# Optimization experiments

Measured on AMD Instinct MI355X. Metric: run time of the kernel, lower is better.

Reference implementation:

```python
import jax, jax.numpy as jnp
import numpy as np

N_NODES = 100000
N_EDGES = 1600000
D_IN, D_HID, D_OUT = 128, 128, 64


def spmm(row, col, val, h, n):
    # y[i] = sum_{e: row[e]==i} val[e] * h[col[e]]  (A_hat @ h with A in COO form)
    return jax.ops.segment_sum(val[:, None] * h[col], row, num_segments=n)


def setup_inputs() -> dict:
    key = jax.random.key(0)
    ks = jax.random.split(key, 7)
    x = jax.random.normal(ks[0], (1, N_NODES, D_IN), dtype=jnp.float32)
    edge_row = jax.random.randint(ks[1], (N_EDGES,), 0, N_NODES, dtype=jnp.int32)
    edge_col = jax.random.randint(ks[2], (N_EDGES,), 0, N_NODES, dtype=jnp.int32)
    edge_val = jax.random.uniform(ks[3], (N_EDGES,), dtype=jnp.float32)
    W0 = jax.random.normal(ks[4], (D_HID, D_IN), dtype=jnp.float32) * 0.05
    W1 = jax.random.normal(ks[5], (D_HID, D_HID), dtype=jnp.float32) * 0.05
    W2 = jax.random.normal(ks[6], (D_OUT, D_HID), dtype=jnp.float32) * 0.05
    return {"x": x, "edge_row": edge_row, "edge_col": edge_col,
            "edge_val": edge_val, "W0": W0, "W1": W1, "W2": W2}


def reference(x, edge_row, edge_col, edge_val, W0, W1, W2):
    B, N, D = x.shape
    n = B * N
    h = x.reshape(n, D)
    # input conv: Linear (no bias) -> SpMM -> ReLU
    h = jax.nn.relu(spmm(edge_row, edge_col, edge_val, h @ W0.T, n))
    # hidden conv with residual: ReLU(A (h W1^T)) + h
    h = jax.nn.relu(spmm(edge_row, edge_col, edge_val, h @ W1.T, n)) + h
    # dropout is identity in eval mode
    out = spmm(edge_row, edge_col, edge_val, h @ W2.T, n)
    return out
```

## Files before the change

kernel.cpp:

```cpp
#include <hip/hip_runtime.h>


typedef unsigned int u32;
typedef unsigned short u16;
typedef __attribute__((ext_vector_type(8))) short bf16x8;
typedef __attribute__((ext_vector_type(4))) float f32x4;

constexpr int NN = 100000;
constexpr int NE = 1600000;
constexpr int RPB = 128;
constexpr int NBUCK = 784;
constexpr int PAD = 100352;
constexpr int BCAP = 2432;
constexpr int EPB = 4096;
constexpr int P1B = (NE + EPB - 1) / EPB;
constexpr int G0B = (NN + 63) / 64;
constexpr int NCB = 13;
constexpr int HB  = 1024;

__device__ __forceinline__ u16 f2bf(float f) {
    u32 x = __float_as_uint(f);
    x += 0x7fffu + ((x >> 16) & 1u);
    return (u16)(x >> 16);
}

__device__ __forceinline__ void wfrag_one(const float* __restrict__ W,
                                          u16* __restrict__ Wf, int total, int i)
{
    if (i < total) {
        const int j    = i & 7;
        const int lane = (i >> 3) & 63;
        const int kc   = (i >> 9) & 3;
        const int ct   = i >> 11;
        const int src  = (ct * 16 + (lane & 15)) * 128 + kc * 32 + (lane >> 4) * 8 + j;
        Wf[i] = f2bf(W[src]);
    }
}

__global__ __launch_bounds__(256)
void wcvt_kernel(const float* __restrict__ W0, const float* __restrict__ W1,
                 const float* __restrict__ W2, u16* __restrict__ wf0,
                 u16* __restrict__ wf1, u16* __restrict__ wf2)
{
    const int i = blockIdx.x * 256 + threadIdx.x;
    wfrag_one(W0, wf0, 128 * 128, i);
    wfrag_one(W1, wf1, 128 * 128, i);
    wfrag_one(W2, wf2, 64 * 128, i);
}

__global__ __launch_bounds__(256)
void k1_kernel(const float* __restrict__ x, const u16* __restrict__ Wf,
               u16* __restrict__ Cb,
               const int* __restrict__ erow, const int* __restrict__ ecol,
               const float* __restrict__ eval,
               int2* __restrict__ part, int* __restrict__ boffs)
{
    __shared__ u16 smem[64 * 136];
    const int tid = threadIdx.x;

    if ((int)blockIdx.x < P1B) {
        int* shist = (int*)smem;
        int* sexcl = shist + HB;
        int* sdat  = sexcl + HB;
        const int blk = blockIdx.x;

        #pragma unroll
        for (int j = 0; j < HB / 256; ++j) shist[j * 256 + tid] = 0;
        __syncthreads();

        const int base = blk * EPB;
        int rr[EPB / 256];
        #pragma unroll
        for (int j = 0; j < EPB / 256; ++j) {
            const int e = base + j * 256 + tid;
            rr[j] = (e < NE) ? erow[e] : -1;
            if (rr[j] >= 0) atomicAdd(&shist[rr[j] >> 7], 1);
        }
        __syncthreads();

        int c[4]; int tsum = 0;
        #pragma unroll
        for (int i = 0; i < 4; ++i) { c[i] = shist[tid * 4 + i]; tsum += c[i]; }
        sdat[tid] = tsum;
        __syncthreads();
        #pragma unroll
        for (int off = 1; off < 256; off <<= 1) {
            const int v = (tid >= off) ? sdat[tid - off] : 0;
            __syncthreads();
            sdat[tid] += v;
            __syncthreads();
        }
        int run = sdat[tid] - tsum;
        #pragma unroll
        for (int i = 0; i < 4; ++i) { sexcl[tid * 4 + i] = run; run += c[i]; }
        __syncthreads();

        for (int b = tid; b < NBUCK; b += 256)
            boffs[(size_t)b * P1B + blk] = sexcl[b];
        if (tid == 0) boffs[(size_t)NBUCK * P1B + blk] = sdat[255];
        __syncthreads();

        #pragma unroll
        for (int j = 0; j < EPB / 256; ++j) {
            const int r = rr[j];
            if (r >= 0) {
                const int e = base + j * 256 + tid;
                const int pos = atomicAdd(&sexcl[r >> 7], 1);
                part[(size_t)blk * EPB + pos] =
                    make_int2(((r & 127) << 17) | ecol[e], __float_as_int(eval[e]));
            }
        }
        return;
    }

    constexpr int RS   = 136;
    constexpr int PADW = 136;
    u16* sA = smem;
    u16* sC = smem;
    const int w    = tid >> 6;
    const int lane = tid & 63;
    const int m    = lane & 15;
    const int q    = lane >> 4;
    const int rowBase = ((int)blockIdx.x - P1B) * 64;

    #pragma unroll
    for (int i = 0; i < 8; ++i) {
        const int g = (i * 256 + tid) * 4;
        const int r = g >> 7, c = g & 127;
        float4 v = make_float4(0.f, 0.f, 0.f, 0.f);
        if (rowBase + r < NN) v = *(const float4*)(x + (size_t)(rowBase + r) * 128 + c);
        u16* d = &sA[r * RS + c];
        d[0] = f2bf(v.x); d[1] = f2bf(v.y); d[2] = f2bf(v.z); d[3] = f2bf(v.w);
    }
    __syncthreads();

    bf16x8 afrag[4];
    #pragma unroll
    for (int kc = 0; kc < 4; ++kc)
        afrag[kc] = *(const bf16x8*)&sA[(w * 16 + m) * RS + kc * 32 + q * 8];
    __syncthreads();

    #pragma unroll
    for (int ct = 0; ct < 8; ++ct) {
        f32x4 acc = {0.f, 0.f, 0.f, 0.f};
        #pragma unroll
        for (int kc = 0; kc < 4; ++kc) {
            const bf16x8 b = *(const bf16x8*)(Wf + (((ct * 4 + kc) * 64) + lane) * 8);
            acc = __builtin_amdgcn_mfma_f32_16x16x32_bf16(afrag[kc], b, acc, 0, 0, 0);
        }
        #pragma unroll
        for (int r = 0; r < 4; ++r)
            sC[(w * 16 + q * 4 + r) * PADW + ct * 16 + m] = f2bf(acc[r]);
    }
    __syncthreads();

    const int g    = lane >> 2;
    const int cb   = (lane & 3) * 32;
    const int grow = rowBase + w * 16 + g;
    if (grow < NN) {
        #pragma unroll
        for (int i = 0; i < 4; ++i) {
            const int4 v = *(const int4*)&sC[(w * 16 + g) * PADW + cb + i * 8];
            *(int4*)(Cb + (size_t)grow * 128 + cb + i * 8) = v;
        }
    }
}

__global__ __launch_bounds__(256)
void part2_kernel(const int* __restrict__ boffs, const int2* __restrict__ part,
                  int* __restrict__ offs, int2* __restrict__ pce)
{
    __shared__ int2 sbuf[BCAP];
    __shared__ int scnt[RPB * NCB];
    __shared__ int slo[512];
    __shared__ int sinc[512];
    __shared__ int sdata[256];
    const int b = blockIdx.x;
    const int tid = threadIdx.x;

    int s0 = 0, s1 = 0;
    for (int k = tid; k < P1B; k += 256) {
        s0 += boffs[(size_t)b * P1B + k];
        s1 += boffs[(size_t)(b + 1) * P1B + k];
    }
    {
        int k = tid;
        int l0 = 0, ln = 0;
        if (k < P1B) {
            l0 = boffs[(size_t)b * P1B + k];
            ln = boffs[(size_t)(b + 1) * P1B + k] - l0;
        }
        slo[k] = l0; sinc[k] = ln;
        k = tid + 256; l0 = 0; ln = 0;
        if (k < P1B) {
            l0 = boffs[(size_t)b * P1B + k];
            ln = boffs[(size_t)(b + 1) * P1B + k] - l0;
        }
        slo[k] = l0; sinc[k] = ln;
    }
    sdata[tid] = s0;
    __syncthreads();
    #pragma unroll
    for (int off = 128; off > 0; off >>= 1) {
        if (tid < off) sdata[tid] += sdata[tid + off];
        __syncthreads();
    }
    const int gb = sdata[0];
    __syncthreads();
    sdata[tid] = s1;
    __syncthreads();
    #pragma unroll
    for (int off = 128; off > 0; off >>= 1) {
        if (tid < off) sdata[tid] += sdata[tid + off];
        __syncthreads();
    }
    const int cnt = sdata[0] - gb;
    __syncthreads();

    for (int j = tid; j < RPB * NCB; j += 256) scnt[j] = 0;
    __syncthreads();

    for (int off = 1; off < 512; off <<= 1) {
        const int v0 = (tid >= off) ? sinc[tid - off] : 0;
        const int v1 = (tid + 256 >= off) ? sinc[tid + 256 - off] : 0;
        __syncthreads();
        sinc[tid]       += v0;
        sinc[tid + 256] += v1;
        __syncthreads();
    }

    for (int i = tid; i < cnt; i += 256) {
        int k = 0;
        #pragma unroll
        for (int step = 256; step > 0; step >>= 1) {
            const int nk = k + step;
            if (nk <= 511 && sinc[nk - 1] <= i) k = nk;
        }
        const int loc = i - (k ? sinc[k - 1] : 0);
        sbuf[i] = part[(size_t)k * EPB + slo[k] + loc];
    }
    __syncthreads();

    for (int i = tid; i < cnt; i += 256) {
        const int xk = sbuf[i].x;
        atomicAdd(&scnt[(((u32)xk) >> 17) * NCB + ((xk & 0x1FFFF) >> 13)], 1);
    }
    __syncthreads();

    int rsum = 0;
    if (tid < RPB) {
        #pragma unroll
        for (int j = 0; j < NCB; ++j) rsum += scnt[tid * NCB + j];
    }
    sdata[tid] = rsum;
    __syncthreads();
    #pragma unroll
    for (int off = 1; off < 256; off <<= 1) {
        const int v = (tid >= off) ? sdata[tid - off] : 0;
        __syncthreads();
        sdata[tid] += v;
        __syncthreads();
    }
    const int excl = sdata[tid] - rsum;
    if (tid < RPB) {
        offs[b * RPB + tid] = gb + excl;
        int run = gb + excl;
        #pragma unroll
        for (int j = 0; j < NCB; ++j) {
            const int c = scnt[tid * NCB + j];
            scnt[tid * NCB + j] = run;
            run += c;
        }
    }
    __syncthreads();

    for (int i = tid; i < cnt; i += 256) {
        const int2 ev = sbuf[i];
        const int pos = atomicAdd(
            &scnt[(((u32)ev.x) >> 17) * NCB + ((ev.x & 0x1FFFF) >> 13)], 1);
        pce[pos] = make_int2(ev.x & 0x1FFFF, ev.y);
    }
}

template<int LPC>
__device__ __forceinline__ void load_row(const u16* p, u32* u) {
    if constexpr (LPC == 8) {
        const uint4 t = *(const uint4*)p;
        u[0] = t.x; u[1] = t.y; u[2] = t.z; u[3] = t.w;
    } else {
        const uint2 t = *(const uint2*)p;
        u[0] = t.x; u[1] = t.y;
    }
}

template<int LPC>
__device__ __forceinline__ void fma_row(float v, const u32* u, float* a) {
    #pragma unroll
    for (int j = 0; j < LPC / 2; ++j) {
        a[2*j]   = fmaf(v, __uint_as_float(u[j] << 16),         a[2*j]);
        a[2*j+1] = fmaf(v, __uint_as_float(u[j] & 0xffff0000u), a[2*j+1]);
    }
}

template<int DO, int MODE>
__global__ __launch_bounds__(256)
void spmm_gemm(const int* __restrict__ offs, const int2* __restrict__ pce,
               const u16* __restrict__ Hb, const u16* __restrict__ Wf,
               const u16* __restrict__ Res, u16* __restrict__ Cb,
               u16* __restrict__ Hout)
{
    constexpr int RS   = 136;
    constexpr int PADW = DO + 8;
    __shared__ u16 smem[16 * 136];
    const int tid = threadIdx.x;
    const int ln  = tid & 15;
    const int rl  = tid >> 4;
    const int row = blockIdx.x * 16 + rl;

    const int s = offs[row];
    const int t = offs[row + 1];
    const u16* hbase = Hb + ln * 8;

    float a0[8], a1[8];
    #pragma unroll
    for (int j = 0; j < 8; ++j) { a0[j] = 0.f; a1[j] = 0.f; }

    for (int e = s; e < t; e += 16) {
        int2 my = make_int2(0, 0);
        if (e + ln < t) my = pce[e + ln];
        const int rem = t - e;
        #pragma unroll
        for (int qd = 0; qd < 4; ++qd) {
            if (qd * 4 < rem) {
                const int c0 = __shfl(my.x, qd * 4 + 0, 16);
                const int v0 = __shfl(my.y, qd * 4 + 0, 16);
                const int c1 = __shfl(my.x, qd * 4 + 1, 16);
                const int v1 = __shfl(my.y, qd * 4 + 1, 16);
                const int c2 = __shfl(my.x, qd * 4 + 2, 16);
                const int v2 = __shfl(my.y, qd * 4 + 2, 16);
                const int c3 = __shfl(my.x, qd * 4 + 3, 16);
                const int v3 = __shfl(my.y, qd * 4 + 3, 16);
                u32 u0[4], u1[4], u2[4], u3[4];
                load_row<8>(hbase + (size_t)c0 * 128, u0);
                load_row<8>(hbase + (size_t)c1 * 128, u1);
                load_row<8>(hbase + (size_t)c2 * 128, u2);
                load_row<8>(hbase + (size_t)c3 * 128, u3);
                fma_row<8>(__int_as_float(v0), u0, a0);
                fma_row<8>(__int_as_float(v1), u1, a1);
                fma_row<8>(__int_as_float(v2), u2, a0);
                fma_row<8>(__int_as_float(v3), u3, a1);
            }
        }
    }
    #pragma unroll
    for (int j = 0; j < 8; ++j) a0[j] = fmaxf(a0[j] + a1[j], 0.f);

    if constexpr (MODE == 2) {
        u32 r[4];
        load_row<8>(Res + (size_t)row * 128 + ln * 8, r);
        #pragma unroll
        for (int j = 0; j < 4; ++j) {
            a0[2*j]   += __uint_as_float(r[j] << 16);
            a0[2*j+1] += __uint_as_float(r[j] & 0xffff0000u);
        }
    }
    u32 o[4];
    #pragma unroll
    for (int j = 0; j < 4; ++j)
        o[j] = (u32)f2bf(a0[2*j]) | ((u32)f2bf(a0[2*j+1]) << 16);
    const uint4 packed = make_uint4(o[0], o[1], o[2], o[3]);
    *(uint4*)&smem[rl * RS + ln * 8] = packed;
    if constexpr (MODE == 1)
        *(uint4*)(Hout + (size_t)row * 128 + ln * 8) = packed;
    __syncthreads();

    constexpr int TPW = DO / 64;
    const int w    = tid >> 6;
    const int lane = tid & 63;
    const int m    = lane & 15;
    const int q    = lane >> 4;

    bf16x8 afrag[4];
    #pragma unroll
    for (int kc = 0; kc < 4; ++kc)
        afrag[kc] = *(const bf16x8*)&smem[m * RS + kc * 32 + q * 8];

    f32x4 acc[TPW];
    #pragma unroll
    for (int tw = 0; tw < TPW; ++tw) {
        const int ct = w * TPW + tw;
        acc[tw] = (f32x4){0.f, 0.f, 0.f, 0.f};
        #pragma unroll
        for (int kc = 0; kc < 4; ++kc) {
            const bf16x8 b = *(const bf16x8*)(Wf + (((ct * 4 + kc) * 64) + lane) * 8);
            acc[tw] = __builtin_amdgcn_mfma_f32_16x16x32_bf16(afrag[kc], b, acc[tw], 0, 0, 0);
        }
    }
    __syncthreads();

    #pragma unroll
    for (int tw = 0; tw < TPW; ++tw) {
        const int ct = w * TPW + tw;
        #pragma unroll
        for (int r = 0; r < 4; ++r)
            smem[(q * 4 + r) * PADW + ct * 16 + m] = f2bf(acc[tw][r]);
    }
    __syncthreads();

    if (DO == 128 || tid < 128) {
        const int g = tid * 8;
        const int r = g / DO;
        const int c = g % DO;
        const int4 v = *(const int4*)&smem[r * PADW + c];
        *(int4*)(Cb + ((size_t)blockIdx.x * 16 + r) * DO + c) = v;
    }
}

__global__ __launch_bounds__(256)
void spmm_out(const int* __restrict__ offs, const int2* __restrict__ pce,
              const u16* __restrict__ Hb, float* __restrict__ Y)
{
    const int ln  = threadIdx.x & 15;
    const int row = blockIdx.x * 16 + (threadIdx.x >> 4);
    if (row >= NN) return;
    const int s = offs[row];
    const int t = offs[row + 1];
    const u16* hbase = Hb + ln * 4;

    float a0[4], a1[4];
    #pragma unroll
    for (int j = 0; j < 4; ++j) { a0[j] = 0.f; a1[j] = 0.f; }

    for (int e = s; e < t; e += 16) {
        int2 my = make_int2(0, 0);
        if (e + ln < t) my = pce[e + ln];
        const int rem = t - e;
        #pragma unroll
        for (int qd = 0; qd < 4; ++qd) {
            if (qd * 4 < rem) {
                const int c0 = __shfl(my.x, qd * 4 + 0, 16);
                const int v0 = __shfl(my.y, qd * 4 + 0, 16);
                const int c1 = __shfl(my.x, qd * 4 + 1, 16);
                const int v1 = __shfl(my.y, qd * 4 + 1, 16);
                const int c2 = __shfl(my.x, qd * 4 + 2, 16);
                const int v2 = __shfl(my.y, qd * 4 + 2, 16);
                const int c3 = __shfl(my.x, qd * 4 + 3, 16);
                const int v3 = __shfl(my.y, qd * 4 + 3, 16);
                u32 u0[2], u1[2], u2[2], u3[2];
                load_row<4>(hbase + (size_t)c0 * 64, u0);
                load_row<4>(hbase + (size_t)c1 * 64, u1);
                load_row<4>(hbase + (size_t)c2 * 64, u2);
                load_row<4>(hbase + (size_t)c3 * 64, u3);
                fma_row<4>(__int_as_float(v0), u0, a0);
                fma_row<4>(__int_as_float(v1), u1, a1);
                fma_row<4>(__int_as_float(v2), u2, a0);
                fma_row<4>(__int_as_float(v3), u3, a1);
            }
        }
    }
    #pragma unroll
    for (int j = 0; j < 4; ++j) a0[j] += a1[j];
    *(float4*)(Y + (size_t)row * 64 + ln * 4) = make_float4(a0[0], a0[1], a0[2], a0[3]);
}

extern "C" void kernel_launch(void* const* d_in, const int* in_sizes, int n_in,
                              void* d_out, int out_size, void* d_ws, size_t ws_size,
                              hipStream_t stream) {
    const float* x    = (const float*)d_in[0];
    const int*   erow = (const int*)  d_in[1];
    const int*   ecol = (const int*)  d_in[2];
    const float* eval = (const float*)d_in[3];
    const float* W0   = (const float*)d_in[4];
    const float* W1   = (const float*)d_in[5];
    const float* W2   = (const float*)d_in[6];
    float* out = (float*)d_out;

    char* p = (char*)d_ws;
    const size_t BUFB = (size_t)NN * 128 * sizeof(u16);
    u16* t0b  = (u16*)p;  p += BUFB;
    u16* t1b  = (u16*)p;  p += BUFB;
    u16* h1b  = (u16*)p;  p += BUFB;
    u16* wf0  = (u16*)p;  p += 128 * 128 * 2;
    u16* wf1  = (u16*)p;  p += 128 * 128 * 2;
    u16* wf2  = (u16*)p;  p += 64 * 128 * 2;
    int* boffs  = (int*)p; p += (size_t)(NBUCK + 1) * P1B * 4;
    int* offs   = (int*)p; p += ((size_t)PAD + 256) * 4;
    int2* part  = (int2*)p; p += (size_t)P1B * EPB * 8;
    int2* pce   = (int2*)p;

    const dim3 blk(256);
    const int rowBlocks = NN / 16;

    wcvt_kernel<<<64, blk, 0, stream>>>(W0, W1, W2, wf0, wf1, wf2);
    k1_kernel  <<<P1B + G0B, blk, 0, stream>>>(x, wf0, t0b, erow, ecol, eval, part, boffs);
    part2_kernel<<<NBUCK, blk, 0, stream>>>(boffs, part, offs, pce);
    spmm_gemm<128, 1><<<rowBlocks, blk, 0, stream>>>(offs, pce, t0b, wf1, nullptr, t1b, h1b);
    spmm_gemm<64, 2><<<rowBlocks, blk, 0, stream>>>(offs, pce, t1b, wf2, h1b, t0b, nullptr);
    spmm_out<<<rowBlocks, blk, 0, stream>>>(offs, pce, t0b, out);
}
```

Before: 319.1 us.

## Widen row buckets to 256, transpose bucket offsets, drop column sub-sort

Edge partitioning now uses 256-row buckets (392 buckets) instead of 128-row buckets, halving the number of part2 blocks and doubling per-block shared capacity. The boffs table is transposed to block-major so phase-1 writes are contiguous, and part2 derives the bucket total from the scan instead of a second reduction. The per-row column sub-bucketing (NCB) is removed, so edges within a row are no longer sorted by column range. This cuts preprocessing work but may reduce gather locality in the SpMM kernels. Larger BCAP risks overflow if a bucket exceeds 4608 edges (expected ~4096).

```diff
diff --git a/kernel.cpp b/kernel.cpp
--- a/kernel.cpp
+++ b/kernel.cpp
@@ -8,15 +8,14 @@
 
 constexpr int NN = 100000;
 constexpr int NE = 1600000;
-constexpr int RPB = 128;
-constexpr int NBUCK = 784;
+constexpr int RPB = 256;
+constexpr int NBUCK = 392;
 constexpr int PAD = 100352;
-constexpr int BCAP = 2432;
+constexpr int BCAP = 4608;
 constexpr int EPB = 4096;
 constexpr int P1B = (NE + EPB - 1) / EPB;
 constexpr int G0B = (NN + 63) / 64;
-constexpr int NCB = 13;
-constexpr int HB  = 1024;
+constexpr int BOS = NBUCK + 1;
 
 __device__ __forceinline__ u16 f2bf(float f) {
     u32 x = __float_as_uint(f);
@@ -60,12 +59,10 @@
 
     if ((int)blockIdx.x < P1B) {
         int* shist = (int*)smem;
-        int* sexcl = shist + HB;
-        int* sdat  = sexcl + HB;
+        int* sexcl = shist + 512;
+        int* sdat  = sexcl + 512;
         const int blk = blockIdx.x;
-
-        #pragma unroll
-        for (int j = 0; j < HB / 256; ++j) shist[j * 256 + tid] = 0;
+        shist[tid] = 0; shist[tid + 256] = 0;
         __syncthreads();
 
         const int base = blk * EPB;
@@ -74,13 +71,13 @@
         for (int j = 0; j < EPB / 256; ++j) {
             const int e = base + j * 256 + tid;
             rr[j] = (e < NE) ? erow[e] : -1;
-            if (rr[j] >= 0) atomicAdd(&shist[rr[j] >> 7], 1);
-        }
-        __syncthreads();
-
-        int c[4]; int tsum = 0;
-        #pragma unroll
-        for (int i = 0; i < 4; ++i) { c[i] = shist[tid * 4 + i]; tsum += c[i]; }
+            if (rr[j] >= 0) atomicAdd(&shist[rr[j] >> 8], 1);
+        }
+        __syncthreads();
+
+        const int c0 = shist[2 * tid];
+        const int c1 = shist[2 * tid + 1];
+        const int tsum = c0 + c1;
         sdat[tid] = tsum;
         __syncthreads();
         #pragma unroll
@@ -90,14 +87,14 @@
             sdat[tid] += v;
             __syncthreads();
         }
-        int run = sdat[tid] - tsum;
-        #pragma unroll
-        for (int i = 0; i < 4; ++i) { sexcl[tid * 4 + i] = run; run += c[i]; }
+        const int excl = sdat[tid] - tsum;
+        sexcl[2 * tid]     = excl;
+        sexcl[2 * tid + 1] = excl + c0;
         __syncthreads();
 
         for (int b = tid; b < NBUCK; b += 256)
-            boffs[(size_t)b * P1B + blk] = sexcl[b];
-        if (tid == 0) boffs[(size_t)NBUCK * P1B + blk] = sdat[255];
+            boffs[(size_t)blk * BOS + b] = sexcl[b];
+        if (tid == 0) boffs[(size_t)blk * BOS + NBUCK] = sdat[255];
         __syncthreads();
 
         #pragma unroll
@@ -105,9 +102,9 @@
             const int r = rr[j];
             if (r >= 0) {
                 const int e = base + j * 256 + tid;
-                const int pos = atomicAdd(&sexcl[r >> 7], 1);
+                const int pos = atomicAdd(&sexcl[r >> 8], 1);
                 part[(size_t)blk * EPB + pos] =
-                    make_int2(((r & 127) << 17) | ecol[e], __float_as_int(eval[e]));
+                    make_int2(((r & 255) << 17) | ecol[e], __float_as_int(eval[e]));
             }
         }
         return;
@@ -171,34 +168,32 @@
                   int* __restrict__ offs, int2* __restrict__ pce)
 {
     __shared__ int2 sbuf[BCAP];
-    __shared__ int scnt[RPB * NCB];
     __shared__ int slo[512];
     __shared__ int sinc[512];
+    __shared__ int scnt[256];
+    __shared__ int rowoff[256];
     __shared__ int sdata[256];
     const int b = blockIdx.x;
     const int tid = threadIdx.x;
 
-    int s0 = 0, s1 = 0;
-    for (int k = tid; k < P1B; k += 256) {
-        s0 += boffs[(size_t)b * P1B + k];
-        s1 += boffs[(size_t)(b + 1) * P1B + k];
-    }
+    int gbp = 0;
     {
         int k = tid;
         int l0 = 0, ln = 0;
         if (k < P1B) {
-            l0 = boffs[(size_t)b * P1B + k];
-            ln = boffs[(size_t)(b + 1) * P1B + k] - l0;
-        }
-        slo[k] = l0; sinc[k] = ln;
+            l0 = boffs[(size_t)k * BOS + b];
+            ln = boffs[(size_t)k * BOS + b + 1] - l0;
+        }
+        slo[k] = l0; sinc[k] = ln; gbp += l0;
         k = tid + 256; l0 = 0; ln = 0;
         if (k < P1B) {
-            l0 = boffs[(size_t)b * P1B + k];
-            ln = boffs[(size_t)(b + 1) * P1B + k] - l0;
-        }
-        slo[k] = l0; sinc[k] = ln;
-    }
-    sdata[tid] = s0;
+            l0 = boffs[(size_t)k * BOS + b];
+            ln = boffs[(size_t)k * BOS + b + 1] - l0;
+        }
+        slo[k] = l0; sinc[k] = ln; gbp += l0;
+    }
+    scnt[tid] = 0;
+    sdata[tid] = gbp;
     __syncthreads();
     #pragma unroll
     for (int off = 128; off > 0; off >>= 1) {
@@ -206,18 +201,6 @@
         __syncthreads();
     }
     const int gb = sdata[0];
-    __syncthreads();
-    sdata[tid] = s1;
-    __syncthreads();
-    #pragma unroll
-    for (int off = 128; off > 0; off >>= 1) {
-        if (tid < off) sdata[tid] += sdata[tid + off];
-        __syncthreads();
-    }
-    const int cnt = sdata[0] - gb;
-    __syncthreads();
-
-    for (int j = tid; j < RPB * NCB; j += 256) scnt[j] = 0;
     __syncthreads();
 
     for (int off = 1; off < 512; off <<= 1) {
@@ -228,6 +211,7 @@
         sinc[tid + 256] += v1;
         __syncthreads();
     }
+    const int cnt = sinc[511];
 
     for (int i = tid; i < cnt; i += 256) {
         int k = 0;
@@ -241,18 +225,12 @@
     }
     __syncthreads();
 
-    for (int i = tid; i < cnt; i += 256) {
-        const int xk = sbuf[i].x;
-        atomicAdd(&scnt[(((u32)xk) >> 17) * NCB + ((xk & 0x1FFFF) >> 13)], 1);
-    }
-    __syncthreads();
-
-    int rsum = 0;
-    if (tid < RPB) {
-        #pragma unroll
-        for (int j = 0; j < NCB; ++j) rsum += scnt[tid * NCB + j];
-    }
-    sdata[tid] = rsum;
+    for (int i = tid; i < cnt; i += 256)
+        atomicAdd(&scnt[((u32)sbuf[i].x) >> 17], 1);
+    __syncthreads();
+
+    const int c = scnt[tid];
+    sdata[tid] = c;
     __syncthreads();
     #pragma unroll
     for (int off = 1; off < 256; off <<= 1) {
@@ -261,23 +239,15 @@
         sdata[tid] += v;
         __syncthreads();
     }
-    const int excl = sdata[tid] - rsum;
-    if (tid < RPB) {
-        offs[b * RPB + tid] = gb + excl;
-        int run = gb + excl;
-        #pragma unroll
-        for (int j = 0; j < NCB; ++j) {
-            const int c = scnt[tid * NCB + j];
-            scnt[tid * NCB + j] = run;
-            run += c;
-        }
-    }
+    const int excl = sdata[tid] - c;
+    offs[b * RPB + tid] = gb + excl;
+    rowoff[tid] = gb + excl;
     __syncthreads();
 
     for (int i = tid; i < cnt; i += 256) {
         const int2 ev = sbuf[i];
-        const int pos = atomicAdd(
-            &scnt[(((u32)ev.x) >> 17) * NCB + ((ev.x & 0x1FFFF) >> 13)], 1);
+        const int rl = ((u32)ev.x) >> 17;
+        const int pos = atomicAdd(&rowoff[rl], 1);
         pce[pos] = make_int2(ev.x & 0x1FFFF, ev.y);
     }
 }
@@ -483,7 +453,7 @@
     u16* wf0  = (u16*)p;  p += 128 * 128 * 2;
     u16* wf1  = (u16*)p;  p += 128 * 128 * 2;
     u16* wf2  = (u16*)p;  p += 64 * 128 * 2;
-    int* boffs  = (int*)p; p += (size_t)(NBUCK + 1) * P1B * 4;
+    int* boffs  = (int*)p; p += (size_t)P1B * BOS * 4;
     int* offs   = (int*)p; p += ((size_t)PAD + 256) * 4;
     int2* part  = (int2*)p; p += (size_t)P1B * EPB * 8;
     int2* pce   = (int2*)p;
```

New measurement: 322.2 us. About the same (+1.0%).
